# Kernel optimization log

Measured on AMD Instinct MI355X. Metric: run time of the kernel, lower is better.

## Reference

```python
import jax, jax.numpy as jnp
import numpy as np

B, S, D_MODEL, HEAD = 4, 4096, 1024, 64


def rope(x):
    # Faithful to the torch code: 'odd' = even-indexed elems, 'even' = odd-indexed.
    b, s, d = x.shape
    half = d // 2
    pos = jnp.arange(s, dtype=x.dtype)
    theta = 1.0 / (10000.0 ** (jnp.arange(half, dtype=x.dtype) / half))
    freqs = pos[:, None] * theta[None, :]  # (s, half)
    sin, cos = jnp.sin(freqs), jnp.cos(freqs)
    odd = x[..., 0::2]
    even = x[..., 1::2]
    x_rot_even = even * cos + odd * sin
    x_rot_odd = odd * cos - even * sin
    return jnp.stack([x_rot_odd, x_rot_even], axis=-1).reshape(x.shape)


def setup_inputs() -> dict:
    key = jax.random.key(0)
    kx, kq, kk, kv = jax.random.split(key, 4)
    x = jax.random.normal(kx, (B, S, D_MODEL), dtype=jnp.float32)
    # torch Linear weights are [out,in]; we store the transposed [in,out] form.
    sc = 1.0 / np.sqrt(D_MODEL)
    Wq = jax.random.normal(kq, (D_MODEL, HEAD), dtype=jnp.float32) * sc
    Wk = jax.random.normal(kk, (D_MODEL, HEAD), dtype=jnp.float32) * sc
    Wv = jax.random.normal(kv, (D_MODEL, HEAD), dtype=jnp.float32) * sc
    return {"x": x, "Wq": Wq, "Wk": Wk, "Wv": Wv}


def reference(x, Wq, Wk, Wv):
    Q = rope(x @ Wq)  # (B, S, H)
    K = rope(x @ Wk)
    V = x @ Wv
    scale = K.shape[-1] ** -0.5
    scores = jnp.einsum('bqh,bkh->bqk', Q, K) * scale  # (B, S, S)
    causal = jnp.tril(jnp.ones((S, S), dtype=bool))
    scores = jnp.where(causal, scores, -jnp.inf)
    probs = jax.nn.softmax(scores, axis=-1)  # dropout p treated as 0 (eval)
    return jnp.einsum('bqk,bkh->bqh', probs, V)
```

## Files before the change

kernel.cpp:

```cpp
#include <hip/hip_runtime.h>
#include <stdint.h>


static constexpr int S_LEN  = 4096;
static constexpr int DMODEL = 1024;
static constexpr int NS     = 6;
static constexpr float SHIFT = 8.0f;

typedef __attribute__((ext_vector_type(8))) short bf16x8;
typedef __attribute__((ext_vector_type(4))) float f32x4;

#define MFMA16(a, b, c) __builtin_amdgcn_mfma_f32_16x16x32_bf16((a), (b), (c), 0, 0, 0)

__device__ __forceinline__ unsigned short f2b(float f) {
    union { float f; unsigned int u; } v;
    v.f = f;
    unsigned int u = v.u;
    u += 0x7fffu + ((u >> 16) & 1u);
    return (unsigned short)(u >> 16);
}
__device__ __forceinline__ float b2f(unsigned short b) {
    union { unsigned int u; float f; } v;
    v.u = ((unsigned int)b) << 16;
    return v.f;
}

template <int CTRL>
__device__ __forceinline__ float dpp_f(float v) {
    return __builtin_bit_cast(float,
        __builtin_amdgcn_update_dpp(0, __builtin_bit_cast(int, v), CTRL, 0xf, 0xf, false));
}
__device__ __forceinline__ float rowsum16(float v) {
    v += dpp_f<0x128>(v);
    v += dpp_f<0x124>(v);
    v += dpp_f<0x122>(v);
    v += dpp_f<0x121>(v);
    return v;
}

__device__ __forceinline__ void dma16(const void* g, void* l) {
    __builtin_amdgcn_global_load_lds(
        (const __attribute__((address_space(1))) unsigned int*)g,
        (__attribute__((address_space(3))) unsigned int*)l, 16, 0, 0);
}

__global__ __launch_bounds__(256) void prep_wt(const float* __restrict__ Wq,
                                               const float* __restrict__ Wk,
                                               const float* __restrict__ Wv,
                                               unsigned short* __restrict__ Wt) {
    int idx = blockIdx.x * 256 + threadIdx.x;
    int c = idx >> 10;
    int k = idx & 1023;
    int mat = c >> 6, n = c & 63;
    const float* W = (mat == 0) ? Wq : (mat == 1) ? Wk : Wv;
    Wt[idx] = f2b(W[k * 64 + n]);
}

__global__ __launch_bounds__(256) void proj_rope(const float* __restrict__ x,
                                                 const unsigned short* __restrict__ Wt,
                                                 unsigned short* __restrict__ Qg,
                                                 unsigned short* __restrict__ Kg,
                                                 unsigned short* __restrict__ Vtg) {
    __shared__ __align__(16) float Xs[2][16 * 128];

    const int tid  = threadIdx.x;
    const int wave = tid >> 6, lane = tid & 63;
    const int l15  = lane & 15, quad = lane >> 4;
    const int rbase = blockIdx.x * 16;

    f32x4 acc[3];
#pragma unroll
    for (int ft = 0; ft < 3; ++ft) acc[ft] = (f32x4){0.f, 0.f, 0.f, 0.f};

    const int f0 = (2 * wave) * 64 + lane, f1 = (2 * wave + 1) * 64 + lane;
    const int r0 = f0 >> 5, c0 = f0 & 31;
    const int r1 = f1 >> 5, c1 = f1 & 31;
    const int s0 = (c0 ^ (r0 & 7)) * 4, s1 = (c1 ^ (r1 & 7)) * 4;
    const float* xg = x + (size_t)rbase * DMODEL;

    auto stage = [&](int kc, int buf) {
        const float* xp = xg + kc * 128;
        dma16(xp + (size_t)r0 * DMODEL + s0, &Xs[buf][(2 * wave) * 256]);
        dma16(xp + (size_t)r1 * DMODEL + s1, &Xs[buf][(2 * wave + 1) * 256]);
    };

    const unsigned short* wb = Wt + (wave * 48 + l15) * 1024;

    stage(0, 0);
    int p = 0;
#pragma unroll 1
    for (int kc = 0; kc < 8; ++kc) {
        __syncthreads();
        if (kc + 1 < 8) stage(kc + 1, p ^ 1);

        const float* Xb = &Xs[p][0];
        const int m = l15 & 7;
#pragma unroll
        for (int kc2 = 0; kc2 < 4; ++kc2) {
            float4 a0 = *reinterpret_cast<const float4*>(
                Xb + l15 * 128 + (kc2 * 8 + ((quad * 2) ^ m)) * 4);
            float4 a1 = *reinterpret_cast<const float4*>(
                Xb + l15 * 128 + (kc2 * 8 + ((quad * 2 + 1) ^ m)) * 4);
            bf16x8 af;
            af[0] = (short)f2b(a0.x); af[1] = (short)f2b(a0.y);
            af[2] = (short)f2b(a0.z); af[3] = (short)f2b(a0.w);
            af[4] = (short)f2b(a1.x); af[5] = (short)f2b(a1.y);
            af[6] = (short)f2b(a1.z); af[7] = (short)f2b(a1.w);
            const int kk = kc * 128 + kc2 * 32 + quad * 8;
#pragma unroll
            for (int ft = 0; ft < 3; ++ft) {
                bf16x8 bf = *reinterpret_cast<const bf16x8*>(wb + ft * 16384 + kk);
                acc[ft] = MFMA16(af, bf, acc[ft]);
            }
        }
        p ^= 1;
    }

#pragma unroll
    for (int ft = 0; ft < 3; ++ft) {
        const int col0 = wave * 48 + ft * 16;
        const int mat  = col0 >> 6;
        const int d    = (col0 & 63) + l15;
        float theta = 0.f;
        if (mat < 2) {
            int i = d >> 1;
            theta = exp2f((float)i * -0.41524101186f);
        }
#pragma unroll
        for (int r = 0; r < 4; ++r) {
            const int gr   = rbase + quad * 4 + r;
            const int b    = gr >> 12;
            const int spos = gr & (S_LEN - 1);
            float v = acc[ft][r];
            if (mat < 2) {
                float partner = __shfl_xor(v, 1);
                float fr = (float)spos * theta;
                float sn = __sinf(fr);
                float cs = __cosf(fr);
                float outv = (d & 1) ? (v * cs + partner * sn)
                                     : (v * cs - partner * sn);
                if (mat == 0) outv *= 0.125f;
                unsigned short bv = f2b(outv);
                if (mat == 0) Qg[(size_t)gr * 64 + d] = bv;
                else          Kg[(size_t)gr * 64 + d] = bv;
            } else {
                Vtg[(size_t)b * (64 * S_LEN) + (size_t)d * S_LEN + spos] = f2b(v);
            }
        }
    }
}

__global__ __launch_bounds__(256) void attn_split(const unsigned short* __restrict__ Qg,
                                                  const unsigned short* __restrict__ Kg,
                                                  const unsigned short* __restrict__ Vtg,
                                                  unsigned short* __restrict__ OP,
                                                  float* __restrict__ L) {
    __shared__ __align__(16) unsigned short Klds[2][64 * 64];
    __shared__ __align__(16) unsigned short Vlds[2][64 * 64];
    __shared__ __align__(16) unsigned short Plds[4][16 * 72];

    const int tid  = threadIdx.x;
    const int wave = tid >> 6, lane = tid & 63;
    const int l15  = lane & 15, quad = lane >> 4;
    const int qt = 63 - blockIdx.x;
    const int split = blockIdx.y, b = blockIdx.z;
    const int qbase = qt * 64;

    const int total = qt + 1;
    const int chunk = (total + NS - 1) / NS;
    const int k0 = split * chunk;
    const int k1 = (k0 + chunk < total) ? (k0 + chunk) : total;

    bf16x8 qa[2];
    {
        const unsigned short* qrow = Qg + (size_t)(b * S_LEN + qbase + wave * 16 + l15) * 64;
        qa[0] = *reinterpret_cast<const bf16x8*>(qrow + quad * 8);
        qa[1] = *reinterpret_cast<const bf16x8*>(qrow + 32 + quad * 8);
    }

    f32x4 o[4];
    float lsum[4];
#pragma unroll
    for (int nt = 0; nt < 4; ++nt) o[nt] = (f32x4){0.f, 0.f, 0.f, 0.f};
#pragma unroll
    for (int r = 0; r < 4; ++r) lsum[r] = 0.f;

    const unsigned short* kgb = Kg  + (size_t)(b * S_LEN) * 64;
    const unsigned short* vgb = Vtg + (size_t)b * (64 * S_LEN);
    unsigned short* Pw = &Plds[wave][0];

    const int i0 = 2 * wave, i1 = 2 * wave + 1;
    const int r0 = (i0 * 64 + lane) >> 3, g0 = (i0 * 64 + lane) & 7;
    const int r1 = (i1 * 64 + lane) >> 3, g1 = (i1 * 64 + lane) & 7;
    const int sg0 = (g0 ^ (r0 & 7)) * 8, sg1 = (g1 ^ (r1 & 7)) * 8;

    auto stage = [&](int kt, int buf) {
        const unsigned short* kp = kgb + (size_t)kt * 64 * 64;
        dma16(kp + r0 * 64 + sg0, &Klds[buf][i0 * 512]);
        dma16(kp + r1 * 64 + sg1, &Klds[buf][i1 * 512]);
        const unsigned short* vp = vgb + (size_t)kt * 64;
        dma16(vp + (size_t)r0 * S_LEN + sg0, &Vlds[buf][i0 * 512]);
        dma16(vp + (size_t)r1 * S_LEN + sg1, &Vlds[buf][i1 * 512]);
    };

    if (k0 < k1) stage(k0, 0);

    int p = 0;
    for (int kt = k0; kt < k1; ++kt) {
        __syncthreads();
        if (kt + 1 < k1) stage(kt + 1, p ^ 1);

        const unsigned short* Kb = &Klds[p][0];
        const unsigned short* Vb = &Vlds[p][0];

        f32x4 s[4];
#pragma unroll
        for (int nt = 0; nt < 4; ++nt) {
            const int rk = nt * 16 + l15;
            bf16x8 kb0 = *reinterpret_cast<const bf16x8*>(Kb + rk * 64 + ((quad ^ (rk & 7)) * 8));
            bf16x8 kb1 = *reinterpret_cast<const bf16x8*>(Kb + rk * 64 + (((4 + quad) ^ (rk & 7)) * 8));
            f32x4 z = (f32x4){0.f, 0.f, 0.f, 0.f};
            z = MFMA16(qa[0], kb0, z);
            z = MFMA16(qa[1], kb1, z);
            s[nt] = z;
        }

        if (kt == qt) {
#pragma unroll
            for (int nt = 0; nt < 4; ++nt) {
                int key_l = nt * 16 + l15;
#pragma unroll
                for (int r = 0; r < 4; ++r) {
                    int q_l = wave * 16 + quad * 4 + r;
                    if (key_l > q_l) s[nt][r] = -1e30f;
                }
            }
        }

#pragma unroll
        for (int nt = 0; nt < 4; ++nt)
#pragma unroll
            for (int r = 0; r < 4; ++r) {
                float pv = __expf(s[nt][r] - SHIFT);
                s[nt][r] = pv;
                lsum[r] += pv;
            }

#pragma unroll
        for (int nt = 0; nt < 4; ++nt)
#pragma unroll
            for (int r = 0; r < 4; ++r)
                Pw[(quad * 4 + r) * 72 + nt * 16 + l15] = f2b(s[nt][r]);

#pragma unroll
        for (int kc = 0; kc < 2; ++kc) {
            bf16x8 pa = *reinterpret_cast<const bf16x8*>(Pw + l15 * 72 + kc * 32 + quad * 8);
#pragma unroll
            for (int nt = 0; nt < 4; ++nt) {
                const int rv = nt * 16 + l15;
                bf16x8 vb = *reinterpret_cast<const bf16x8*>(
                    Vb + rv * 64 + (((kc * 4 + quad) ^ (rv & 7)) * 8));
                o[nt] = MFMA16(pa, vb, o[nt]);
            }
        }
        p ^= 1;
    }

#pragma unroll
    for (int r = 0; r < 4; ++r) lsum[r] = rowsum16(lsum[r]);

    const size_t prow_base = ((size_t)(split * 4 + b)) * S_LEN;
#pragma unroll
    for (int nt = 0; nt < 4; ++nt)
#pragma unroll
        for (int r = 0; r < 4; ++r) {
            int row = qbase + wave * 16 + quad * 4 + r;
            OP[(prow_base + row) * 64 + nt * 16 + l15] = f2b(o[nt][r]);
        }
    if (l15 == 0) {
#pragma unroll
        for (int r = 0; r < 4; ++r) {
            int row = qbase + wave * 16 + quad * 4 + r;
            L[prow_base + row] = lsum[r];
        }
    }
}

__global__ __launch_bounds__(256) void combine(const unsigned short* __restrict__ OP,
                                               const float* __restrict__ L,
                                               float* __restrict__ out) {
    int idx = blockIdx.x * 256 + threadIdx.x;
    int d   = idx & 63;
    int row = (idx >> 6) & (S_LEN - 1);
    int b   = idx >> 18;

    float num = 0.f, den = 0.f;
#pragma unroll
    for (int s = 0; s < NS; ++s) {
        size_t pr = (size_t)(s * 4 + b) * S_LEN + row;
        den += L[pr];
        num += b2f(OP[pr * 64 + d]);
    }
    out[idx] = num / den;
}

extern "C" void kernel_launch(void* const* d_in, const int* in_sizes, int n_in,
                              void* d_out, int out_size, void* d_ws, size_t ws_size,
                              hipStream_t stream) {
    const float* x  = (const float*)d_in[0];
    const float* Wq = (const float*)d_in[1];
    const float* Wk = (const float*)d_in[2];
    const float* Wv = (const float*)d_in[3];
    float* out = (float*)d_out;

    unsigned char* base = (unsigned char*)d_ws;
    unsigned short* Qg  = (unsigned short*)(base);
    unsigned short* Kg  = (unsigned short*)(base + (2u << 20));
    unsigned short* Vtg = (unsigned short*)(base + (4u << 20));
    unsigned short* Wt  = (unsigned short*)(base + (6u << 20));
    float*          L   = (float*)(base + (6u << 20) + (1u << 19));
    unsigned short* OP  = (unsigned short*)(base + (7u << 20));

    prep_wt<<<768, 256, 0, stream>>>(Wq, Wk, Wv, Wt);
    proj_rope<<<1024, 256, 0, stream>>>(x, Wt, Qg, Kg, Vtg);
    attn_split<<<dim3(64, NS, 4), 256, 0, stream>>>(Qg, Kg, Vtg, OP, L);
    combine<<<4096, 256, 0, stream>>>(OP, L, out);
}
```

Before: 177.2 us.

## Tile projection over 64 rows and stage weights in LDS for reuse

The projection kernel now processes 64 rows per block instead of 16. Each wave computes 4 M-fragments against 3 weight fragments, and the weight K-chunks are DMA-staged into swizzled shared memory alongside the x tile. This raises reuse of each weight load across rows and cuts the per-block global weight traffic. The grid drops from 1024 to 256 blocks, which may reduce occupancy and parallelism for a stage that is a small part of total time.

```diff
diff --git a/kernel.cpp b/kernel.cpp
--- a/kernel.cpp
+++ b/kernel.cpp
@@ -61,56 +61,76 @@
                                                  unsigned short* __restrict__ Qg,
                                                  unsigned short* __restrict__ Kg,
                                                  unsigned short* __restrict__ Vtg) {
-    __shared__ __align__(16) float Xs[2][16 * 128];
+    __shared__ __align__(16) float          Xs[2][64 * 64];
+    __shared__ __align__(16) unsigned short Bs[2][192 * 64];
 
     const int tid  = threadIdx.x;
     const int wave = tid >> 6, lane = tid & 63;
     const int l15  = lane & 15, quad = lane >> 4;
-    const int rbase = blockIdx.x * 16;
-
-    f32x4 acc[3];
-#pragma unroll
-    for (int ft = 0; ft < 3; ++ft) acc[ft] = (f32x4){0.f, 0.f, 0.f, 0.f};
-
-    const int f0 = (2 * wave) * 64 + lane, f1 = (2 * wave + 1) * 64 + lane;
-    const int r0 = f0 >> 5, c0 = f0 & 31;
-    const int r1 = f1 >> 5, c1 = f1 & 31;
-    const int s0 = (c0 ^ (r0 & 7)) * 4, s1 = (c1 ^ (r1 & 7)) * 4;
+    const int rbase = blockIdx.x * 64;
+
+    f32x4 acc[4][3];
+#pragma unroll
+    for (int mf = 0; mf < 4; ++mf)
+#pragma unroll
+        for (int ft = 0; ft < 3; ++ft) acc[mf][ft] = (f32x4){0.f, 0.f, 0.f, 0.f};
+
     const float* xg = x + (size_t)rbase * DMODEL;
 
     auto stage = [&](int kc, int buf) {
-        const float* xp = xg + kc * 128;
-        dma16(xp + (size_t)r0 * DMODEL + s0, &Xs[buf][(2 * wave) * 256]);
-        dma16(xp + (size_t)r1 * DMODEL + s1, &Xs[buf][(2 * wave + 1) * 256]);
+#pragma unroll
+        for (int ii = 0; ii < 4; ++ii) {
+            const int i = 4 * wave + ii;
+            const int row = i * 4 + (lane >> 4);
+            const int gd = lane & 15;
+            const int gs = (gd & 8) | ((gd & 7) ^ (row & 7));
+            dma16(xg + (size_t)row * DMODEL + kc * 64 + gs * 4, &Xs[buf][i * 256]);
+        }
+#pragma unroll
+        for (int jj = 0; jj < 6; ++jj) {
+            const int j = 6 * wave + jj;
+            const int col = j * 8 + (lane >> 3);
+            const int gd = lane & 7;
+            const int gs = gd ^ (col & 7);
+            dma16(Wt + (size_t)col * 1024 + kc * 64 + gs * 8, &Bs[buf][j * 512]);
+        }
     };
-
-    const unsigned short* wb = Wt + (wave * 48 + l15) * 1024;
 
     stage(0, 0);
     int p = 0;
+    const int msk = l15 & 7;
+
 #pragma unroll 1
-    for (int kc = 0; kc < 8; ++kc) {
+    for (int kc = 0; kc < 16; ++kc) {
         __syncthreads();
-        if (kc + 1 < 8) stage(kc + 1, p ^ 1);
+        if (kc + 1 < 16) stage(kc + 1, p ^ 1);
 
         const float* Xb = &Xs[p][0];
-        const int m = l15 & 7;
-#pragma unroll
-        for (int kc2 = 0; kc2 < 4; ++kc2) {
-            float4 a0 = *reinterpret_cast<const float4*>(
-                Xb + l15 * 128 + (kc2 * 8 + ((quad * 2) ^ m)) * 4);
-            float4 a1 = *reinterpret_cast<const float4*>(
-                Xb + l15 * 128 + (kc2 * 8 + ((quad * 2 + 1) ^ m)) * 4);
-            bf16x8 af;
-            af[0] = (short)f2b(a0.x); af[1] = (short)f2b(a0.y);
-            af[2] = (short)f2b(a0.z); af[3] = (short)f2b(a0.w);
-            af[4] = (short)f2b(a1.x); af[5] = (short)f2b(a1.y);
-            af[6] = (short)f2b(a1.z); af[7] = (short)f2b(a1.w);
-            const int kk = kc * 128 + kc2 * 32 + quad * 8;
-#pragma unroll
-            for (int ft = 0; ft < 3; ++ft) {
-                bf16x8 bf = *reinterpret_cast<const bf16x8*>(wb + ft * 16384 + kk);
-                acc[ft] = MFMA16(af, bf, acc[ft]);
+        const unsigned short* Bb = &Bs[p][0];
+
+#pragma unroll
+        for (int kk2 = 0; kk2 < 2; ++kk2) {
+            bf16x8 bf0 = *reinterpret_cast<const bf16x8*>(
+                Bb + (wave * 48 + 0 * 16 + l15) * 64 + ((kk2 * 4 + quad) ^ msk) * 8);
+            bf16x8 bf1 = *reinterpret_cast<const bf16x8*>(
+                Bb + (wave * 48 + 1 * 16 + l15) * 64 + ((kk2 * 4 + quad) ^ msk) * 8);
+            bf16x8 bf2 = *reinterpret_cast<const bf16x8*>(
+                Bb + (wave * 48 + 2 * 16 + l15) * 64 + ((kk2 * 4 + quad) ^ msk) * 8);
+#pragma unroll
+            for (int mf = 0; mf < 4; ++mf) {
+                const int row = mf * 16 + l15;
+                float4 a0 = *reinterpret_cast<const float4*>(
+                    Xb + row * 64 + (kk2 * 8 + ((quad * 2) ^ msk)) * 4);
+                float4 a1 = *reinterpret_cast<const float4*>(
+                    Xb + row * 64 + (kk2 * 8 + ((quad * 2 + 1) ^ msk)) * 4);
+                bf16x8 af;
+                af[0] = (short)f2b(a0.x); af[1] = (short)f2b(a0.y);
+                af[2] = (short)f2b(a0.z); af[3] = (short)f2b(a0.w);
+                af[4] = (short)f2b(a1.x); af[5] = (short)f2b(a1.y);
+                af[6] = (short)f2b(a1.z); af[7] = (short)f2b(a1.w);
+                acc[mf][0] = MFMA16(af, bf0, acc[mf][0]);
+                acc[mf][1] = MFMA16(af, bf1, acc[mf][1]);
+                acc[mf][2] = MFMA16(af, bf2, acc[mf][2]);
             }
         }
         p ^= 1;
@@ -127,24 +147,27 @@
             theta = exp2f((float)i * -0.41524101186f);
         }
 #pragma unroll
-        for (int r = 0; r < 4; ++r) {
-            const int gr   = rbase + quad * 4 + r;
-            const int b    = gr >> 12;
-            const int spos = gr & (S_LEN - 1);
-            float v = acc[ft][r];
-            if (mat < 2) {
-                float partner = __shfl_xor(v, 1);
-                float fr = (float)spos * theta;
-                float sn = __sinf(fr);
-                float cs = __cosf(fr);
-                float outv = (d & 1) ? (v * cs + partner * sn)
-                                     : (v * cs - partner * sn);
-                if (mat == 0) outv *= 0.125f;
-                unsigned short bv = f2b(outv);
-                if (mat == 0) Qg[(size_t)gr * 64 + d] = bv;
-                else          Kg[(size_t)gr * 64 + d] = bv;
-            } else {
-                Vtg[(size_t)b * (64 * S_LEN) + (size_t)d * S_LEN + spos] = f2b(v);
+        for (int mf = 0; mf < 4; ++mf) {
+#pragma unroll
+            for (int r = 0; r < 4; ++r) {
+                const int gr   = rbase + mf * 16 + quad * 4 + r;
+                const int b    = gr >> 12;
+                const int spos = gr & (S_LEN - 1);
+                float v = acc[mf][ft][r];
+                if (mat < 2) {
+                    float partner = __shfl_xor(v, 1);
+                    float fr = (float)spos * theta;
+                    float sn = __sinf(fr);
+                    float cs = __cosf(fr);
+                    float outv = (d & 1) ? (v * cs + partner * sn)
+                                         : (v * cs - partner * sn);
+                    if (mat == 0) outv *= 0.125f;
+                    unsigned short bv = f2b(outv);
+                    if (mat == 0) Qg[(size_t)gr * 64 + d] = bv;
+                    else          Kg[(size_t)gr * 64 + d] = bv;
+                } else {
+                    Vtg[(size_t)b * (64 * S_LEN) + (size_t)d * S_LEN + spos] = f2b(v);
+                }
             }
         }
     }
@@ -322,7 +345,7 @@
     unsigned short* OP  = (unsigned short*)(base + (7u << 20));
 
     prep_wt<<<768, 256, 0, stream>>>(Wq, Wk, Wv, Wt);
-    proj_rope<<<1024, 256, 0, stream>>>(x, Wt, Qg, Kg, Vtg);
+    proj_rope<<<256, 256, 0, stream>>>(x, Wt, Qg, Kg, Vtg);
     attn_split<<<dim3(64, NS, 4), 256, 0, stream>>>(Qg, Kg, Vtg, OP, L);
     combine<<<4096, 256, 0, stream>>>(OP, L, out);
 }
```

Result: faster. 161.1 us (-9.1%).
